# Optimization experiments

Hardware: AMD Instinct MI355X
Metric: run time of the kernel (lower is better)

## Reference

```python
import jax, jax.numpy as jnp
import numpy as np

N = 50000        # nodes
E = 800000       # edges (avg degree 16)
C = 64           # node_dim = mid_planes = out_planes
EDGE_DIM = 16    # edge feature dim
S = 8            # share_planes


def setup_inputs() -> dict:
    key = jax.random.key(0)
    ks = jax.random.split(key, 20)

    def lin_w(k, fin, fout):
        return (jax.random.normal(k, (fin, fout), jnp.float32) / np.sqrt(fin)).astype(jnp.float32)

    return {
        "q": jax.random.normal(ks[0], (N, C), jnp.float32),
        "k": jax.random.normal(ks[1], (N, C), jnp.float32),
        "v": jax.random.normal(ks[2], (N, C), jnp.float32),
        "edges": jax.random.normal(ks[3], (E, EDGE_DIM), jnp.float32),
        "edge_index": jax.random.randint(ks[4], (E, 2), 0, N, jnp.int32),
        # linear_q / linear_k / linear_v : C -> C
        "Wq": lin_w(ks[5], C, C), "bq": jnp.zeros((C,), jnp.float32),
        "Wk": lin_w(ks[6], C, C), "bk": jnp.zeros((C,), jnp.float32),
        "Wv": lin_w(ks[7], C, C), "bv": jnp.zeros((C,), jnp.float32),
        # linear_p : EDGE_DIM -> 1
        "Wp": lin_w(ks[8], EDGE_DIM, 1), "bp": jnp.zeros((1,), jnp.float32),
        # linear_w : ReLU -> Linear(C, C//S) -> ReLU -> Linear(C//S, C//S)
        "W1": lin_w(ks[9], C, C // S), "b1": jnp.zeros((C // S,), jnp.float32),
        "W2": lin_w(ks[10], C // S, C // S), "b2": jnp.zeros((C // S,), jnp.float32),
    }


def reference(q, k, v, edges, edge_index,
              Wq, bq, Wk, bk, Wv, bv, Wp, bp, W1, b1, W2, b2):
    src = edge_index[:, 0]  # destination node of aggregation (query side)
    dst = edge_index[:, 1]  # neighbor node (key/value side)

    # node-level projections, then gather per edge
    x_q = (q @ Wq + bq)[src]            # [E, C]
    x_k = (k @ Wk + bk)[dst]            # [E, C]
    x_v = (v @ Wv + bv)[dst]            # [E, C]

    p_r = edges @ Wp + bp               # [E, 1] positional bias

    # vector attention weights (per-edge MLP)
    w = x_k - x_q + p_r                 # [E, C]
    w = jax.nn.relu(w) @ W1 + b1        # [E, C//S]
    w = jax.nn.relu(w) @ W2 + b2        # [E, C//S]
    w = jax.nn.softmax(w, axis=1)       # softmax over shared channel groups

    # weighted values, grouped by share_planes, scatter-sum back to nodes
    msg = ((x_v + p_r).reshape(E, S, C // S) * w[:, None, :]).reshape(E, C)
    return jax.ops.segment_sum(msg, src, num_segments=N)  # [N, C]
```

## Files before the change

kernel.cpp:

```cpp
#include <hip/hip_runtime.h>
#include <hip/hip_fp16.h>

#define N_NODES 50000
#define E_EDGES 800000
#define SCAN_TILE 1024
#define SCAN_NBLK ((N_NODES + SCAN_TILE - 1) / SCAN_TILE)
#define EW_EPT 4

__device__ __forceinline__ float sgpr_f(float x) {
    return __uint_as_float(__builtin_amdgcn_readfirstlane(__float_as_uint(x)));
}

#if defined(__has_builtin)
#if __has_builtin(__builtin_amdgcn_fdot2)
#define HAS_FDOT2 1
#endif
#endif

typedef _Float16 v2h_t __attribute__((ext_vector_type(2)));

__device__ __forceinline__ float fdot2f(__half2 a, __half2 b, float c) {
#ifdef HAS_FDOT2
    return __builtin_amdgcn_fdot2(*reinterpret_cast<v2h_t*>(&a),
                                  *reinterpret_cast<v2h_t*>(&b), c, false);
#else
    const float2 fa = __half22float2(a);
    const float2 fb = __half22float2(b);
    return fmaf(fa.x, fb.x, fmaf(fa.y, fb.y, c));
#endif
}

__device__ __forceinline__ __half2 relu_h2(__half2 x) {
    union { __half2 h; unsigned u; } a, r;
    a.h = x;
    asm("v_pk_max_f16 %0, %1, 0" : "=v"(r.u) : "v"(a.u));
    return r.h;
}

template <int CTRL>
__device__ __forceinline__ float dpp_mov_f32(float x) {
    return __int_as_float(__builtin_amdgcn_update_dpp(
        0, __float_as_int(x), CTRL, 0xF, 0xF, true));
}
__device__ __forceinline__ float oct_sum(float x) {
    x += dpp_mov_f32<0xB1>(x);
    x += dpp_mov_f32<0x4E>(x);
    x += dpp_mov_f32<0x141>(x);
    return x;
}
__device__ __forceinline__ float oct_max(float x) {
    x = fmaxf(x, dpp_mov_f32<0xB1>(x));
    x = fmaxf(x, dpp_mov_f32<0x4E>(x));
    x = fmaxf(x, dpp_mov_f32<0x141>(x));
    return x;
}

__global__ __launch_bounds__(256) void proj_kernel(
    const float* __restrict__ qin, const float* __restrict__ kin, const float* __restrict__ vin,
    const float* __restrict__ Wq, const float* __restrict__ bq,
    const float* __restrict__ Wk, const float* __restrict__ bk,
    const float* __restrict__ Wv, const float* __restrict__ bv,
    __half* __restrict__ xq, __half* __restrict__ xk, __half* __restrict__ xv)
{
    __shared__ float Ws[3 * 4096];
    const int tid = threadIdx.x;
    #pragma unroll
    for (int it = 0; it < 16; ++it) {
        const int idx = it * 256 + tid;
        Ws[idx]        = Wq[idx];
        Ws[4096 + idx] = Wk[idx];
        Ws[8192 + idx] = Wv[idx];
    }
    __syncthreads();

    const int cg = tid & 15;
    const int rg = tid >> 4;
    const int c0 = cg * 4;
    const int base = blockIdx.x * 64 + rg * 4;

    const float* ins[3]  = {qin, kin, vin};
    const float* bs[3]   = {bq, bk, bv};
    __half*      outs[3] = {xq, xk, xv};

    int rowi[4];
    #pragma unroll
    for (int rr = 0; rr < 4; ++rr)
        rowi[rr] = (base + rr < N_NODES) ? (base + rr) : (N_NODES - 1);

    #pragma unroll
    for (int m = 0; m < 3; ++m) {
        const float* in = ins[m];
        const float* Wm = &Ws[m * 4096];
        float4 acc[4];
        const float4 b4 = *reinterpret_cast<const float4*>(&bs[m][c0]);
        #pragma unroll
        for (int rr = 0; rr < 4; ++rr) acc[rr] = b4;

        for (int kk = 0; kk < 64; kk += 4) {
            float4 rv[4];
            #pragma unroll
            for (int rr = 0; rr < 4; ++rr)
                rv[rr] = *reinterpret_cast<const float4*>(&in[rowi[rr] * 64 + kk]);
            #pragma unroll
            for (int dk = 0; dk < 4; ++dk) {
                const float4 w4 = *reinterpret_cast<const float4*>(&Wm[(kk + dk) * 64 + c0]);
                #pragma unroll
                for (int rr = 0; rr < 4; ++rr) {
                    const float xs = reinterpret_cast<const float*>(&rv[rr])[dk];
                    acc[rr].x = fmaf(xs, w4.x, acc[rr].x);
                    acc[rr].y = fmaf(xs, w4.y, acc[rr].y);
                    acc[rr].z = fmaf(xs, w4.z, acc[rr].z);
                    acc[rr].w = fmaf(xs, w4.w, acc[rr].w);
                }
            }
        }
        #pragma unroll
        for (int rr = 0; rr < 4; ++rr) {
            if (base + rr < N_NODES) {
                union { __half2 h[2]; uint2 u; } pk;
                pk.h[0] = __floats2half2_rn(acc[rr].x, acc[rr].y);
                pk.h[1] = __floats2half2_rn(acc[rr].z, acc[rr].w);
                *reinterpret_cast<uint2*>(&outs[m][(size_t)(base + rr) * 64 + c0]) = pk.u;
            }
        }
    }
}

__global__ __launch_bounds__(256) void scan_sums(
    const int* __restrict__ cnt, int* __restrict__ bsum)
{
    const int tid  = threadIdx.x;
    const int base = blockIdx.x * SCAN_TILE + tid * 4;
    int s = 0;
    if (base + 3 < N_NODES) {
        const int4 t = *reinterpret_cast<const int4*>(&cnt[base]);
        s = t.x + t.y + t.z + t.w;
    } else {
        #pragma unroll
        for (int i = 0; i < 4; ++i)
            if (base + i < N_NODES) s += cnt[base + i];
    }
    #pragma unroll
    for (int d = 1; d < 64; d <<= 1) s += __shfl_xor(s, d);
    __shared__ int ws[4];
    if ((tid & 63) == 0) ws[tid >> 6] = s;
    __syncthreads();
    if (tid == 0) bsum[blockIdx.x] = ws[0] + ws[1] + ws[2] + ws[3];
}

__global__ __launch_bounds__(64) void scan_bsum(int* __restrict__ bsum)
{
    const int lane = threadIdx.x;
    const int v = (lane < SCAN_NBLK) ? bsum[lane] : 0;
    int incl = v;
    #pragma unroll
    for (int d = 1; d < 64; d <<= 1) {
        const int t = __shfl_up(incl, d);
        if (lane >= d) incl += t;
    }
    if (lane < SCAN_NBLK) bsum[lane] = incl - v;
}

__global__ __launch_bounds__(256) void scan_final(
    int* __restrict__ cnt, const int* __restrict__ bsum, int* __restrict__ off)
{
    const int tid  = threadIdx.x;
    const int base = blockIdx.x * SCAN_TILE + tid * 4;

    int v0 = 0, v1 = 0, v2 = 0, v3 = 0;
    if (base + 3 < N_NODES) {
        const int4 t = *reinterpret_cast<const int4*>(&cnt[base]);
        v0 = t.x; v1 = t.y; v2 = t.z; v3 = t.w;
    } else {
        if (base + 0 < N_NODES) v0 = cnt[base + 0];
        if (base + 1 < N_NODES) v1 = cnt[base + 1];
        if (base + 2 < N_NODES) v2 = cnt[base + 2];
        if (base + 3 < N_NODES) v3 = cnt[base + 3];
    }
    const int s = v0 + v1 + v2 + v3;

    int incl = s;
    #pragma unroll
    for (int d = 1; d < 64; d <<= 1) {
        const int t = __shfl_up(incl, d);
        if ((tid & 63) >= d) incl += t;
    }
    __shared__ int wsum[4];
    const int wave = tid >> 6;
    if ((tid & 63) == 63) wsum[wave] = incl;
    __syncthreads();
    int woff = 0;
    #pragma unroll
    for (int w = 0; w < 3; ++w)
        if (w < wave) woff += wsum[w];

    int run = bsum[blockIdx.x] + woff + (incl - s);
    if (base + 0 < N_NODES) { off[base + 0] = run; cnt[base + 0] = run; run += v0; }
    if (base + 1 < N_NODES) { off[base + 1] = run; cnt[base + 1] = run; run += v1; }
    if (base + 2 < N_NODES) { off[base + 2] = run; cnt[base + 2] = run; run += v2; }
    if (base + 3 < N_NODES) { off[base + 3] = run; cnt[base + 3] = run; run += v3; }

    if (blockIdx.x == 0 && tid == 0) off[N_NODES] = E_EDGES;
}

__global__ __launch_bounds__(256) void edge_weights(
    const int* __restrict__ eidx, const float* __restrict__ edges,
    const float* __restrict__ Wp, const float* __restrict__ bp,
    const float* __restrict__ W1, const float* __restrict__ b1,
    const float* __restrict__ W2, const float* __restrict__ b2,
    const __half* __restrict__ xq, const __half* __restrict__ xk,
    int* __restrict__ cnt, float2* __restrict__ ep2e, ushort* __restrict__ wout16)
{
    const int tid  = threadIdx.x;
    const int lane = tid & 63;
    const int o    = lane >> 3;
    const int r    = lane & 7;
    const int wave = tid >> 6;

    __half2 W1h[4][8];
    #pragma unroll
    for (int i = 0; i < 4; ++i) {
        const float4 a0 = *reinterpret_cast<const float4*>(&W1[(8 * r + 2 * i) * 8]);
        const float4 a1 = *reinterpret_cast<const float4*>(&W1[(8 * r + 2 * i) * 8 + 4]);
        const float4 c0 = *reinterpret_cast<const float4*>(&W1[(8 * r + 2 * i + 1) * 8]);
        const float4 c1 = *reinterpret_cast<const float4*>(&W1[(8 * r + 2 * i + 1) * 8 + 4]);
        W1h[i][0] = __floats2half2_rn(a0.x, c0.x);
        W1h[i][1] = __floats2half2_rn(a0.y, c0.y);
        W1h[i][2] = __floats2half2_rn(a0.z, c0.z);
        W1h[i][3] = __floats2half2_rn(a0.w, c0.w);
        W1h[i][4] = __floats2half2_rn(a1.x, c1.x);
        W1h[i][5] = __floats2half2_rn(a1.y, c1.y);
        W1h[i][6] = __floats2half2_rn(a1.z, c1.z);
        W1h[i][7] = __floats2half2_rn(a1.w, c1.w);
    }
    float W2col[8];
    #pragma unroll
    for (int jj = 0; jj < 8; ++jj) W2col[jj] = W2[jj * 8 + r];
    float b1u[8];
    #pragma unroll
    for (int j = 0; j < 8; ++j) b1u[j] = sgpr_f(b1[j]);
    const float b2r = b2[r];
    const float wpA = Wp[2 * r], wpB = Wp[2 * r + 1];
    const float bp0 = sgpr_f(bp[0]);

    const int wb = (blockIdx.x * 4 + wave) * (8 * EW_EPT);

    #pragma unroll
    for (int t = 0; t < EW_EPT; ++t) {
        const int e = wb + t * 8 + o;

        const int2 sd = *reinterpret_cast<const int2*>(&eidx[2 * e]);
        const float2 e2 = *reinterpret_cast<const float2*>(&edges[(size_t)e * 16 + 2 * r]);

        uint4 q4u = *reinterpret_cast<const uint4*>(&xq[(size_t)sd.x * 64 + 8 * r]);
        uint4 k4u = *reinterpret_cast<const uint4*>(&xk[(size_t)sd.y * 64 + 8 * r]);

        float p = fmaf(e2.x, wpA, e2.y * wpB);
        p = oct_sum(p) + bp0;

        const __half2 p2 = __float2half2_rn(p);
        const __half2* qh = reinterpret_cast<const __half2*>(&q4u);
        const __half2* kh = reinterpret_cast<const __half2*>(&k4u);

        float part[8];
        #pragma unroll
        for (int jj = 0; jj < 8; ++jj) part[jj] = 0.f;
        #pragma unroll
        for (int i = 0; i < 4; ++i) {
            const __half2 d = relu_h2(__hadd2(__hsub2(kh[i], qh[i]), p2));
            #pragma unroll
            for (int jj = 0; jj < 8; ++jj)
                part[jj] = fdot2f(d, W1h[i][jj], part[jj]);
        }
        #pragma unroll
        for (int jj = 0; jj < 8; ++jj) part[jj] = oct_sum(part[jj]);

        float h2 = b2r;
        #pragma unroll
        for (int jj = 0; jj < 8; ++jj) {
            const float h1 = fmaxf(part[jj] + b1u[jj], 0.f);
            h2 = fmaf(h1, W2col[jj], h2);
        }

        const float mx = oct_max(h2);
        const float ex = __expf(h2 - mx);
        const float s  = oct_sum(ex);
        const float w  = ex / s;

        wout16[(size_t)e * 8 + r] = __half_as_ushort(__float2half_rn(w));
        if (r == 0) ep2e[e] = make_float2(p, __int_as_float(sd.y));
        if (r == 1) atomicAdd(&cnt[sd.x], 1);
    }
}

__global__ __launch_bounds__(256) void scatter_kernel(
    const int* __restrict__ eidx, const float2* __restrict__ ep2e,
    const uint4* __restrict__ woute,
    int* __restrict__ cursor, float2* __restrict__ ep2, uint4* __restrict__ wcsr)
{
    const int e = blockIdx.x * 256 + threadIdx.x;
    const int src = eidx[2 * e];
    const float2 ep = ep2e[e];
    const uint4 w8 = woute[e];

    const int pos = atomicAdd(&cursor[src], 1);
    ep2[pos]  = ep;
    wcsr[pos] = w8;
}

__global__ __launch_bounds__(256) void node_accum(
    const int* __restrict__ off, const float2* __restrict__ ep2,
    const uint4* __restrict__ wcsr, const __half* __restrict__ xv,
    float* __restrict__ out)
{
    const int tid  = threadIdx.x;
    const int lane = tid & 63;
    const int grp  = lane >> 4;
    const int sub  = (lane >> 3) & 1;
    const int r    = lane & 7;
    const int wave = tid >> 6;

    const int node = blockIdx.x * 16 + wave * 4 + grp;

    const int beg = off[node];
    const int end = off[node + 1];

    float acc[8];
    #pragma unroll
    for (int i = 0; i < 8; ++i) acc[i] = 0.f;

    int j = beg + sub;
    float2 ep;
    uint4  w8;
    if (j < end) { ep = ep2[j]; w8 = wcsr[j]; }

    for (; j < end; j += 2) {
        const float p   = ep.x;
        const int   dst = __float_as_int(ep.y);

        union { uint4 u; __half2 h[4]; } v4, wz;
        v4.u = *reinterpret_cast<const uint4*>(&xv[(size_t)dst * 64 + 8 * r]);
        wz.u = w8;

        if (j + 2 < end) { ep = ep2[j + 2]; w8 = wcsr[j + 2]; }

        #pragma unroll
        for (int i = 0; i < 4; ++i) {
            const float2 fv = __half22float2(v4.h[i]);
            const float2 fw = __half22float2(wz.h[i]);
            acc[2 * i]     = fmaf(fv.x + p, fw.x, acc[2 * i]);
            acc[2 * i + 1] = fmaf(fv.y + p, fw.y, acc[2 * i + 1]);
        }
    }

    #pragma unroll
    for (int i = 0; i < 8; ++i)
        acc[i] += __shfl_xor(acc[i], 8);

    if (sub == 0) {
        float* orow = &out[(size_t)node * 64 + 8 * r];
        *reinterpret_cast<float4*>(orow)     = make_float4(acc[0], acc[1], acc[2], acc[3]);
        *reinterpret_cast<float4*>(orow + 4) = make_float4(acc[4], acc[5], acc[6], acc[7]);
    }
}

extern "C" void kernel_launch(void* const* d_in, const int* in_sizes, int n_in,
                              void* d_out, int out_size, void* d_ws, size_t ws_size,
                              hipStream_t stream) {
    const float* q     = (const float*)d_in[0];
    const float* k     = (const float*)d_in[1];
    const float* v     = (const float*)d_in[2];
    const float* edges = (const float*)d_in[3];
    const int*   eidx  = (const int*)d_in[4];
    const float* Wq    = (const float*)d_in[5];
    const float* bq    = (const float*)d_in[6];
    const float* Wk    = (const float*)d_in[7];
    const float* bk    = (const float*)d_in[8];
    const float* Wv    = (const float*)d_in[9];
    const float* bv    = (const float*)d_in[10];
    const float* Wp    = (const float*)d_in[11];
    const float* bp    = (const float*)d_in[12];
    const float* W1    = (const float*)d_in[13];
    const float* b1    = (const float*)d_in[14];
    const float* W2    = (const float*)d_in[15];
    const float* b2    = (const float*)d_in[16];
    float* out = (float*)d_out;

    char* ws = (char*)d_ws;
    __half* xq = (__half*)ws;          ws += (size_t)N_NODES * 64 * sizeof(__half);
    __half* xk = (__half*)ws;          ws += (size_t)N_NODES * 64 * sizeof(__half);
    __half* xv = (__half*)ws;          ws += (size_t)N_NODES * 64 * sizeof(__half);
    int* cnt  = (int*)ws;              ws += (size_t)(N_NODES + 64) * sizeof(int);
    int* off  = (int*)ws;              ws += (size_t)(N_NODES + 64) * sizeof(int);
    int* bsum = (int*)ws;              ws += (size_t)64 * sizeof(int);
    float2* ep2e = (float2*)ws;        ws += (size_t)E_EDGES * sizeof(float2);
    ushort* wout = (ushort*)ws;        ws += (size_t)E_EDGES * 8 * sizeof(ushort);
    float2* ep2  = (float2*)ws;        ws += (size_t)E_EDGES * sizeof(float2);
    uint4*  wcsr = (uint4*)ws;         ws += (size_t)E_EDGES * sizeof(uint4);

    hipMemsetAsync(cnt, 0, (size_t)N_NODES * sizeof(int), stream);

    proj_kernel<<<dim3((N_NODES + 63) / 64), dim3(256), 0, stream>>>(
        q, k, v, Wq, bq, Wk, bk, Wv, bv, xq, xk, xv);

    edge_weights<<<dim3(E_EDGES / (32 * EW_EPT)), dim3(256), 0, stream>>>(
        eidx, edges, Wp, bp, W1, b1, W2, b2, xq, xk, cnt, ep2e, wout);

    scan_sums<<<dim3(SCAN_NBLK), dim3(256), 0, stream>>>(cnt, bsum);
    scan_bsum<<<dim3(1), dim3(64), 0, stream>>>(bsum);
    scan_final<<<dim3(SCAN_NBLK), dim3(256), 0, stream>>>(cnt, bsum, off);

    scatter_kernel<<<dim3(E_EDGES / 256), dim3(256), 0, stream>>>(
        eidx, ep2e, (const uint4*)wout, cnt, ep2, wcsr);

    node_accum<<<dim3(N_NODES / 16), dim3(256), 0, stream>>>(
        off, ep2, wcsr, xv, out);
}
```

Measured before the change: 187.4 us.

## Fuse edge-weight MLP into CSR node accumulation with interleaved K/V rows

Moves the per-edge attention MLP and softmax out of a separate edge-ordered kernel and into the node-ordered accumulation kernel. Each node now loads its query once, and each neighbour's K and V are fetched together from one interleaved row. This removes the intermediate per-edge weight buffer and its scatter into CSR order. A lightweight histogram kernel and a scatter kernel that computes only the positional bias take its place. In exchange, each lane computes all 8 second-layer outputs redundantly and the sequential per-node loop carries more arithmetic, which adds register pressure and latency.

```diff
diff --git a/kernel.cpp b/kernel.cpp
--- a/kernel.cpp
+++ b/kernel.cpp
@@ -5,7 +5,6 @@
 #define E_EDGES 800000
 #define SCAN_TILE 1024
 #define SCAN_NBLK ((N_NODES + SCAN_TILE - 1) / SCAN_TILE)
-#define EW_EPT 4
 
 __device__ __forceinline__ float sgpr_f(float x) {
     return __uint_as_float(__builtin_amdgcn_readfirstlane(__float_as_uint(x)));
@@ -48,19 +47,13 @@
     x += dpp_mov_f32<0x141>(x);
     return x;
 }
-__device__ __forceinline__ float oct_max(float x) {
-    x = fmaxf(x, dpp_mov_f32<0xB1>(x));
-    x = fmaxf(x, dpp_mov_f32<0x4E>(x));
-    x = fmaxf(x, dpp_mov_f32<0x141>(x));
-    return x;
-}
 
 __global__ __launch_bounds__(256) void proj_kernel(
     const float* __restrict__ qin, const float* __restrict__ kin, const float* __restrict__ vin,
     const float* __restrict__ Wq, const float* __restrict__ bq,
     const float* __restrict__ Wk, const float* __restrict__ bk,
     const float* __restrict__ Wv, const float* __restrict__ bv,
-    __half* __restrict__ xq, __half* __restrict__ xk, __half* __restrict__ xv)
+    __half* __restrict__ xq, __half* __restrict__ xkv)
 {
     __shared__ float Ws[3 * 4096];
     const int tid = threadIdx.x;
@@ -78,9 +71,8 @@
     const int c0 = cg * 4;
     const int base = blockIdx.x * 64 + rg * 4;
 
-    const float* ins[3]  = {qin, kin, vin};
-    const float* bs[3]   = {bq, bk, bv};
-    __half*      outs[3] = {xq, xk, xv};
+    const float* ins[3] = {qin, kin, vin};
+    const float* bs[3]  = {bq, bk, bv};
 
     int rowi[4];
     #pragma unroll
@@ -120,10 +112,21 @@
                 union { __half2 h[2]; uint2 u; } pk;
                 pk.h[0] = __floats2half2_rn(acc[rr].x, acc[rr].y);
                 pk.h[1] = __floats2half2_rn(acc[rr].z, acc[rr].w);
-                *reinterpret_cast<uint2*>(&outs[m][(size_t)(base + rr) * 64 + c0]) = pk.u;
+                __half* obase;
+                if (m == 0)      obase = &xq[(size_t)(base + rr) * 64 + c0];
+                else if (m == 1) obase = &xkv[(size_t)(base + rr) * 128 + c0];
+                else             obase = &xkv[(size_t)(base + rr) * 128 + 64 + c0];
+                *reinterpret_cast<uint2*>(obase) = pk.u;
             }
         }
     }
+}
+
+__global__ __launch_bounds__(256) void hist_kernel(
+    const int* __restrict__ eidx, int* __restrict__ cnt)
+{
+    const int e = blockIdx.x * 256 + threadIdx.x;
+    atomicAdd(&cnt[eidx[2 * e]], 1);
 }
 
 __global__ __launch_bounds__(256) void scan_sums(
@@ -203,17 +206,41 @@
     if (blockIdx.x == 0 && tid == 0) off[N_NODES] = E_EDGES;
 }
 
-__global__ __launch_bounds__(256) void edge_weights(
+__global__ __launch_bounds__(256) void scatter_p(
     const int* __restrict__ eidx, const float* __restrict__ edges,
     const float* __restrict__ Wp, const float* __restrict__ bp,
+    int* __restrict__ cursor, float2* __restrict__ ep2)
+{
+    const int e = blockIdx.x * 256 + threadIdx.x;
+    const int src = eidx[2 * e];
+    const int dst = eidx[2 * e + 1];
+
+    float pr = bp[0];
+    #pragma unroll
+    for (int q4 = 0; q4 < 4; ++q4) {
+        const float4 ev = *reinterpret_cast<const float4*>(&edges[(size_t)e * 16 + q4 * 4]);
+        const float4 wv = *reinterpret_cast<const float4*>(&Wp[q4 * 4]);
+        pr = fmaf(ev.x, wv.x, pr);
+        pr = fmaf(ev.y, wv.y, pr);
+        pr = fmaf(ev.z, wv.z, pr);
+        pr = fmaf(ev.w, wv.w, pr);
+    }
+
+    const int pos = atomicAdd(&cursor[src], 1);
+    ep2[pos] = make_float2(pr, __int_as_float(dst));
+}
+
+__global__ __launch_bounds__(256) void node_fused(
+    const int* __restrict__ off, const float2* __restrict__ ep2,
     const float* __restrict__ W1, const float* __restrict__ b1,
     const float* __restrict__ W2, const float* __restrict__ b2,
-    const __half* __restrict__ xq, const __half* __restrict__ xk,
-    int* __restrict__ cnt, float2* __restrict__ ep2e, ushort* __restrict__ wout16)
+    const __half* __restrict__ xq, const __half* __restrict__ xkv,
+    float* __restrict__ out)
 {
     const int tid  = threadIdx.x;
     const int lane = tid & 63;
-    const int o    = lane >> 3;
+    const int grp  = lane >> 4;
+    const int sub  = (lane >> 3) & 1;
     const int r    = lane & 7;
     const int wave = tid >> 6;
 
@@ -233,123 +260,90 @@
         W1h[i][6] = __floats2half2_rn(a1.z, c1.z);
         W1h[i][7] = __floats2half2_rn(a1.w, c1.w);
     }
-    float W2col[8];
-    #pragma unroll
-    for (int jj = 0; jj < 8; ++jj) W2col[jj] = W2[jj * 8 + r];
-    float b1u[8];
-    #pragma unroll
-    for (int j = 0; j < 8; ++j) b1u[j] = sgpr_f(b1[j]);
-    const float b2r = b2[r];
-    const float wpA = Wp[2 * r], wpB = Wp[2 * r + 1];
-    const float bp0 = sgpr_f(bp[0]);
-
-    const int wb = (blockIdx.x * 4 + wave) * (8 * EW_EPT);
-
-    #pragma unroll
-    for (int t = 0; t < EW_EPT; ++t) {
-        const int e = wb + t * 8 + o;
-
-        const int2 sd = *reinterpret_cast<const int2*>(&eidx[2 * e]);
-        const float2 e2 = *reinterpret_cast<const float2*>(&edges[(size_t)e * 16 + 2 * r]);
-
-        uint4 q4u = *reinterpret_cast<const uint4*>(&xq[(size_t)sd.x * 64 + 8 * r]);
-        uint4 k4u = *reinterpret_cast<const uint4*>(&xk[(size_t)sd.y * 64 + 8 * r]);
-
-        float p = fmaf(e2.x, wpA, e2.y * wpB);
-        p = oct_sum(p) + bp0;
-
-        const __half2 p2 = __float2half2_rn(p);
-        const __half2* qh = reinterpret_cast<const __half2*>(&q4u);
-        const __half2* kh = reinterpret_cast<const __half2*>(&k4u);
-
-        float part[8];
+    float W2u[8][8];
+    #pragma unroll
+    for (int jj = 0; jj < 8; ++jj)
         #pragma unroll
-        for (int jj = 0; jj < 8; ++jj) part[jj] = 0.f;
-        #pragma unroll
-        for (int i = 0; i < 4; ++i) {
-            const __half2 d = relu_h2(__hadd2(__hsub2(kh[i], qh[i]), p2));
-            #pragma unroll
-            for (int jj = 0; jj < 8; ++jj)
-                part[jj] = fdot2f(d, W1h[i][jj], part[jj]);
-        }
-        #pragma unroll
-        for (int jj = 0; jj < 8; ++jj) part[jj] = oct_sum(part[jj]);
-
-        float h2 = b2r;
-        #pragma unroll
-        for (int jj = 0; jj < 8; ++jj) {
-            const float h1 = fmaxf(part[jj] + b1u[jj], 0.f);
-            h2 = fmaf(h1, W2col[jj], h2);
-        }
-
-        const float mx = oct_max(h2);
-        const float ex = __expf(h2 - mx);
-        const float s  = oct_sum(ex);
-        const float w  = ex / s;
-
-        wout16[(size_t)e * 8 + r] = __half_as_ushort(__float2half_rn(w));
-        if (r == 0) ep2e[e] = make_float2(p, __int_as_float(sd.y));
-        if (r == 1) atomicAdd(&cnt[sd.x], 1);
-    }
-}
-
-__global__ __launch_bounds__(256) void scatter_kernel(
-    const int* __restrict__ eidx, const float2* __restrict__ ep2e,
-    const uint4* __restrict__ woute,
-    int* __restrict__ cursor, float2* __restrict__ ep2, uint4* __restrict__ wcsr)
-{
-    const int e = blockIdx.x * 256 + threadIdx.x;
-    const int src = eidx[2 * e];
-    const float2 ep = ep2e[e];
-    const uint4 w8 = woute[e];
-
-    const int pos = atomicAdd(&cursor[src], 1);
-    ep2[pos]  = ep;
-    wcsr[pos] = w8;
-}
-
-__global__ __launch_bounds__(256) void node_accum(
-    const int* __restrict__ off, const float2* __restrict__ ep2,
-    const uint4* __restrict__ wcsr, const __half* __restrict__ xv,
-    float* __restrict__ out)
-{
-    const int tid  = threadIdx.x;
-    const int lane = tid & 63;
-    const int grp  = lane >> 4;
-    const int sub  = (lane >> 3) & 1;
-    const int r    = lane & 7;
-    const int wave = tid >> 6;
+        for (int j2 = 0; j2 < 8; ++j2)
+            W2u[jj][j2] = sgpr_f(W2[jj * 8 + j2]);
+    float b1u[8], b2u[8];
+    #pragma unroll
+    for (int j2 = 0; j2 < 8; ++j2) { b1u[j2] = sgpr_f(b1[j2]); b2u[j2] = sgpr_f(b2[j2]); }
 
     const int node = blockIdx.x * 16 + wave * 4 + grp;
 
     const int beg = off[node];
     const int end = off[node + 1];
 
+    uint4 q4u = *reinterpret_cast<const uint4*>(&xq[(size_t)node * 64 + 8 * r]);
+    const __half2* qh = reinterpret_cast<const __half2*>(&q4u);
+
     float acc[8];
     #pragma unroll
     for (int i = 0; i < 8; ++i) acc[i] = 0.f;
 
     int j = beg + sub;
-    float2 ep;
-    uint4  w8;
-    if (j < end) { ep = ep2[j]; w8 = wcsr[j]; }
-
-    for (; j < end; j += 2) {
-        const float p   = ep.x;
-        const int   dst = __float_as_int(ep.y);
-
-        union { uint4 u; __half2 h[4]; } v4, wz;
-        v4.u = *reinterpret_cast<const uint4*>(&xv[(size_t)dst * 64 + 8 * r]);
-        wz.u = w8;
-
-        if (j + 2 < end) { ep = ep2[j + 2]; w8 = wcsr[j + 2]; }
-
-        #pragma unroll
-        for (int i = 0; i < 4; ++i) {
-            const float2 fv = __half22float2(v4.h[i]);
-            const float2 fw = __half22float2(wz.h[i]);
-            acc[2 * i]     = fmaf(fv.x + p, fw.x, acc[2 * i]);
-            acc[2 * i + 1] = fmaf(fv.y + p, fw.y, acc[2 * i + 1]);
+    if (j < end) {
+        float2 e0 = ep2[j];
+        const int jc1 = (j + 2 < end) ? (j + 2) : (end - 1);
+        float2 e1 = ep2[jc1];
+        size_t gb = (size_t)__float_as_int(e0.y) * 128 + 8 * r;
+        uint4 k4 = *reinterpret_cast<const uint4*>(&xkv[gb]);
+        uint4 v4 = *reinterpret_cast<const uint4*>(&xkv[gb + 64]);
+
+        for (; j < end; j += 2) {
+            const size_t gbn = (size_t)__float_as_int(e1.y) * 128 + 8 * r;
+            uint4 k4n = *reinterpret_cast<const uint4*>(&xkv[gbn]);
+            uint4 v4n = *reinterpret_cast<const uint4*>(&xkv[gbn + 64]);
+            const int jc2 = (j + 4 < end) ? (j + 4) : (end - 1);
+            float2 e2r = ep2[jc2];
+
+            const float p = e0.x;
+            const __half2 p2 = __float2half2_rn(p);
+            const __half2* kh = reinterpret_cast<const __half2*>(&k4);
+
+            float part[8];
+            #pragma unroll
+            for (int jj = 0; jj < 8; ++jj) part[jj] = 0.f;
+            #pragma unroll
+            for (int i = 0; i < 4; ++i) {
+                const __half2 d = relu_h2(__hadd2(__hsub2(kh[i], qh[i]), p2));
+                #pragma unroll
+                for (int jj = 0; jj < 8; ++jj)
+                    part[jj] = fdot2f(d, W1h[i][jj], part[jj]);
+            }
+            #pragma unroll
+            for (int jj = 0; jj < 8; ++jj) part[jj] = oct_sum(part[jj]);
+
+            float g[8];
+            #pragma unroll
+            for (int jj = 0; jj < 8; ++jj) g[jj] = fmaxf(part[jj] + b1u[jj], 0.f);
+            float h2[8];
+            #pragma unroll
+            for (int j2 = 0; j2 < 8; ++j2) h2[j2] = b2u[j2];
+            #pragma unroll
+            for (int jj = 0; jj < 8; ++jj)
+                #pragma unroll
+                for (int j2 = 0; j2 < 8; ++j2)
+                    h2[j2] = fmaf(g[jj], W2u[jj][j2], h2[j2]);
+
+            float mx = h2[0];
+            #pragma unroll
+            for (int j2 = 1; j2 < 8; ++j2) mx = fmaxf(mx, h2[j2]);
+            float ex[8], s = 0.f;
+            #pragma unroll
+            for (int j2 = 0; j2 < 8; ++j2) { ex[j2] = __expf(h2[j2] - mx); s += ex[j2]; }
+            const float inv = 1.f / s;
+
+            const __half2* vh = reinterpret_cast<const __half2*>(&v4);
+            #pragma unroll
+            for (int i = 0; i < 4; ++i) {
+                const float2 fv = __half22float2(vh[i]);
+                acc[2 * i]     = fmaf(fv.x + p, ex[2 * i] * inv,     acc[2 * i]);
+                acc[2 * i + 1] = fmaf(fv.y + p, ex[2 * i + 1] * inv, acc[2 * i + 1]);
+            }
+
+            e0 = e1; e1 = e2r; k4 = k4n; v4 = v4n;
         }
     }
 
@@ -387,32 +381,27 @@
     float* out = (float*)d_out;
 
     char* ws = (char*)d_ws;
-    __half* xq = (__half*)ws;          ws += (size_t)N_NODES * 64 * sizeof(__half);
-    __half* xk = (__half*)ws;          ws += (size_t)N_NODES * 64 * sizeof(__half);
-    __half* xv = (__half*)ws;          ws += (size_t)N_NODES * 64 * sizeof(__half);
+    __half* xq  = (__half*)ws;         ws += (size_t)N_NODES * 64 * sizeof(__half);
+    __half* xkv = (__half*)ws;         ws += (size_t)N_NODES * 128 * sizeof(__half);
     int* cnt  = (int*)ws;              ws += (size_t)(N_NODES + 64) * sizeof(int);
     int* off  = (int*)ws;              ws += (size_t)(N_NODES + 64) * sizeof(int);
     int* bsum = (int*)ws;              ws += (size_t)64 * sizeof(int);
-    float2* ep2e = (float2*)ws;        ws += (size_t)E_EDGES * sizeof(float2);
-    ushort* wout = (ushort*)ws;        ws += (size_t)E_EDGES * 8 * sizeof(ushort);
-    float2* ep2  = (float2*)ws;        ws += (size_t)E_EDGES * sizeof(float2);
-    uint4*  wcsr = (uint4*)ws;         ws += (size_t)E_EDGES * sizeof(uint4);
+    float2* ep2 = (float2*)ws;         ws += (size_t)E_EDGES * sizeof(float2);
 
     hipMemsetAsync(cnt, 0, (size_t)N_NODES * sizeof(int), stream);
 
-    proj_kernel<<<dim3((N_NODES + 63) / 64), dim3(256), 0, stream>>>(
-        q, k, v, Wq, bq, Wk, bk, Wv, bv, xq, xk, xv);
-
-    edge_weights<<<dim3(E_EDGES / (32 * EW_EPT)), dim3(256), 0, stream>>>(
-        eidx, edges, Wp, bp, W1, b1, W2, b2, xq, xk, cnt, ep2e, wout);
+    hist_kernel<<<dim3(E_EDGES / 256), dim3(256), 0, stream>>>(eidx, cnt);
 
     scan_sums<<<dim3(SCAN_NBLK), dim3(256), 0, stream>>>(cnt, bsum);
     scan_bsum<<<dim3(1), dim3(64), 0, stream>>>(bsum);
     scan_final<<<dim3(SCAN_NBLK), dim3(256), 0, stream>>>(cnt, bsum, off);
 
-    scatter_kernel<<<dim3(E_EDGES / 256), dim3(256), 0, stream>>>(
-        eidx, ep2e, (const uint4*)wout, cnt, ep2, wcsr);
-
-    node_accum<<<dim3(N_NODES / 16), dim3(256), 0, stream>>>(
-        off, ep2, wcsr, xv, out);
-}
+    scatter_p<<<dim3(E_EDGES / 256), dim3(256), 0, stream>>>(
+        eidx, edges, Wp, bp, cnt, ep2);
+
+    proj_kernel<<<dim3((N_NODES + 63) / 64), dim3(256), 0, stream>>>(
+        q, k, v, Wq, bq, Wk, bk, Wv, bv, xq, xkv);
+
+    node_fused<<<dim3(N_NODES / 16), dim3(256), 0, stream>>>(
+        off, ep2, W1, b1, W2, b2, xq, xkv, out);
+}
```

Result: slower. 205.6 us (+9.7%).

## Pack per-edge src/dst, 8-bit weights and bias into one 16-byte record

Applied to the files above, without the earlier changes.

Quantizes the eight softmax weights to 8-bit fixed point, gathers them across lanes with DPP, and packs them with 16-bit src/dst indices and the float positional bias into a single uint4 per edge. The scatter and accumulation kernels then move one 16-byte record instead of separate float2 and uint4 arrays, and the scatter no longer reads edge_index. The intent is to cut memory traffic in the scatter and node_accum stages. The cost is much lower weight precision, and the 16-bit index packing only holds because N is below 65536.

```diff
diff --git a/kernel.cpp b/kernel.cpp
--- a/kernel.cpp
+++ b/kernel.cpp
@@ -41,6 +41,10 @@
 __device__ __forceinline__ float dpp_mov_f32(float x) {
     return __int_as_float(__builtin_amdgcn_update_dpp(
         0, __float_as_int(x), CTRL, 0xF, 0xF, true));
+}
+template <int CTRL>
+__device__ __forceinline__ int dpp_mov_i32(int x) {
+    return __builtin_amdgcn_update_dpp(0, x, CTRL, 0xF, 0xF, true);
 }
 __device__ __forceinline__ float oct_sum(float x) {
     x += dpp_mov_f32<0xB1>(x);
@@ -209,7 +213,7 @@
     const float* __restrict__ W1, const float* __restrict__ b1,
     const float* __restrict__ W2, const float* __restrict__ b2,
     const __half* __restrict__ xq, const __half* __restrict__ xk,
-    int* __restrict__ cnt, float2* __restrict__ ep2e, ushort* __restrict__ wout16)
+    int* __restrict__ cnt, uint4* __restrict__ rece)
 {
     const int tid  = threadIdx.x;
     const int lane = tid & 63;
@@ -284,34 +288,41 @@
 
         const float mx = oct_max(h2);
         const float ex = __expf(h2 - mx);
-        const float s  = oct_sum(ex);
-        const float w  = ex / s;
-
-        wout16[(size_t)e * 8 + r] = __half_as_ushort(__float2half_rn(w));
-        if (r == 0) ep2e[e] = make_float2(p, __int_as_float(sd.y));
+        const float sm = oct_sum(ex);
+        const float w  = ex / sm;
+
+        const unsigned wu = (unsigned)__float2uint_rn(w * 255.f);
+        unsigned word = wu << (8 * (r & 3));
+        word |= (unsigned)dpp_mov_i32<0xB1>((int)word);
+        word |= (unsigned)dpp_mov_i32<0x4E>((int)word);
+        const unsigned other = (unsigned)dpp_mov_i32<0x141>((int)word);
+
+        if (r == 0) {
+            uint4 rec;
+            rec.x = (unsigned)sd.x | ((unsigned)sd.y << 16);
+            rec.y = word;
+            rec.z = other;
+            rec.w = __float_as_uint(p);
+            rece[e] = rec;
+        }
         if (r == 1) atomicAdd(&cnt[sd.x], 1);
     }
 }
 
 __global__ __launch_bounds__(256) void scatter_kernel(
-    const int* __restrict__ eidx, const float2* __restrict__ ep2e,
-    const uint4* __restrict__ woute,
-    int* __restrict__ cursor, float2* __restrict__ ep2, uint4* __restrict__ wcsr)
+    const uint4* __restrict__ rece, int* __restrict__ cursor,
+    uint4* __restrict__ reccsr)
 {
     const int e = blockIdx.x * 256 + threadIdx.x;
-    const int src = eidx[2 * e];
-    const float2 ep = ep2e[e];
-    const uint4 w8 = woute[e];
-
+    const uint4 rec = rece[e];
+    const int src = (int)(rec.x & 0xFFFFu);
     const int pos = atomicAdd(&cursor[src], 1);
-    ep2[pos]  = ep;
-    wcsr[pos] = w8;
+    reccsr[pos] = rec;
 }
 
 __global__ __launch_bounds__(256) void node_accum(
-    const int* __restrict__ off, const float2* __restrict__ ep2,
-    const uint4* __restrict__ wcsr, const __half* __restrict__ xv,
-    float* __restrict__ out)
+    const int* __restrict__ off, const uint4* __restrict__ reccsr,
+    const __half* __restrict__ xv, float* __restrict__ out)
 {
     const int tid  = threadIdx.x;
     const int lane = tid & 63;
@@ -330,26 +341,31 @@
     for (int i = 0; i < 8; ++i) acc[i] = 0.f;
 
     int j = beg + sub;
-    float2 ep;
-    uint4  w8;
-    if (j < end) { ep = ep2[j]; w8 = wcsr[j]; }
+    uint4 rec;
+    if (j < end) rec = reccsr[j];
 
     for (; j < end; j += 2) {
-        const float p   = ep.x;
-        const int   dst = __float_as_int(ep.y);
-
-        union { uint4 u; __half2 h[4]; } v4, wz;
+        const uint4 cur = rec;
+        const int   dst = (int)(cur.x >> 16);
+        const float p   = __uint_as_float(cur.w);
+
+        union { uint4 u; __half2 h[4]; } v4;
         v4.u = *reinterpret_cast<const uint4*>(&xv[(size_t)dst * 64 + 8 * r]);
-        wz.u = w8;
-
-        if (j + 2 < end) { ep = ep2[j + 2]; w8 = wcsr[j + 2]; }
+
+        if (j + 2 < end) rec = reccsr[j + 2];
+
+        float wf[8];
+        #pragma unroll
+        for (int i = 0; i < 4; ++i) {
+            wf[i]     = (float)((cur.y >> (8 * i)) & 255u);
+            wf[4 + i] = (float)((cur.z >> (8 * i)) & 255u);
+        }
 
         #pragma unroll
         for (int i = 0; i < 4; ++i) {
             const float2 fv = __half22float2(v4.h[i]);
-            const float2 fw = __half22float2(wz.h[i]);
-            acc[2 * i]     = fmaf(fv.x + p, fw.x, acc[2 * i]);
-            acc[2 * i + 1] = fmaf(fv.y + p, fw.y, acc[2 * i + 1]);
+            acc[2 * i]     = fmaf(fv.x + p, wf[2 * i],     acc[2 * i]);
+            acc[2 * i + 1] = fmaf(fv.y + p, wf[2 * i + 1], acc[2 * i + 1]);
         }
     }
 
@@ -358,9 +374,12 @@
         acc[i] += __shfl_xor(acc[i], 8);
 
     if (sub == 0) {
+        const float c = 1.f / 255.f;
         float* orow = &out[(size_t)node * 64 + 8 * r];
-        *reinterpret_cast<float4*>(orow)     = make_float4(acc[0], acc[1], acc[2], acc[3]);
-        *reinterpret_cast<float4*>(orow + 4) = make_float4(acc[4], acc[5], acc[6], acc[7]);
+        *reinterpret_cast<float4*>(orow) =
+            make_float4(acc[0] * c, acc[1] * c, acc[2] * c, acc[3] * c);
+        *reinterpret_cast<float4*>(orow + 4) =
+            make_float4(acc[4] * c, acc[5] * c, acc[6] * c, acc[7] * c);
     }
 }
 
@@ -393,10 +412,8 @@
     int* cnt  = (int*)ws;              ws += (size_t)(N_NODES + 64) * sizeof(int);
     int* off  = (int*)ws;              ws += (size_t)(N_NODES + 64) * sizeof(int);
     int* bsum = (int*)ws;              ws += (size_t)64 * sizeof(int);
-    float2* ep2e = (float2*)ws;        ws += (size_t)E_EDGES * sizeof(float2);
-    ushort* wout = (ushort*)ws;        ws += (size_t)E_EDGES * 8 * sizeof(ushort);
-    float2* ep2  = (float2*)ws;        ws += (size_t)E_EDGES * sizeof(float2);
-    uint4*  wcsr = (uint4*)ws;         ws += (size_t)E_EDGES * sizeof(uint4);
+    uint4* rece   = (uint4*)ws;        ws += (size_t)E_EDGES * sizeof(uint4);
+    uint4* reccsr = (uint4*)ws;        ws += (size_t)E_EDGES * sizeof(uint4);
 
     hipMemsetAsync(cnt, 0, (size_t)N_NODES * sizeof(int), stream);
 
@@ -404,15 +421,15 @@
         q, k, v, Wq, bq, Wk, bk, Wv, bv, xq, xk, xv);
 
     edge_weights<<<dim3(E_EDGES / (32 * EW_EPT)), dim3(256), 0, stream>>>(
-        eidx, edges, Wp, bp, W1, b1, W2, b2, xq, xk, cnt, ep2e, wout);
+        eidx, edges, Wp, bp, W1, b1, W2, b2, xq, xk, cnt, rece);
 
     scan_sums<<<dim3(SCAN_NBLK), dim3(256), 0, stream>>>(cnt, bsum);
     scan_bsum<<<dim3(1), dim3(64), 0, stream>>>(bsum);
     scan_final<<<dim3(SCAN_NBLK), dim3(256), 0, stream>>>(cnt, bsum, off);
 
     scatter_kernel<<<dim3(E_EDGES / 256), dim3(256), 0, stream>>>(
-        eidx, ep2e, (const uint4*)wout, cnt, ep2, wcsr);
+        rece, cnt, reccsr);
 
     node_accum<<<dim3(N_NODES / 16), dim3(256), 0, stream>>>(
-        off, ep2, wcsr, xv, out);
-}
+        off, reccsr, xv, out);
+}
```

Result: faster. 181.6 us (-3.1%).
